# Optimization experiments

Hardware: AMD Instinct MI355X
Metric: run time of the kernel (lower is better)

The kernel has to match this reference:

```python
import jax, jax.numpy as jnp
import numpy as np

CELU_ALPHA = 3.0  # hardcoded in the torch module (nn.CELU(alpha=3.0), F.celu(alpha=3.0))

def celu(x):
    # celu(x, a) = max(0, x) + min(0, a*(exp(x/a)-1)); overflow-safe form
    return jnp.maximum(x, 0.0) + CELU_ALPHA * jnp.expm1(jnp.minimum(x, 0.0) / CELU_ALPHA)

def setup_inputs() -> dict:
    key = jax.random.key(0)
    k1, k2, k3, k4, k5 = jax.random.split(key, 5)
    N, E, H, D = 16384, 262144, 4, 64
    return {
        "features": jax.random.normal(k1, (N, D), dtype=jnp.float32),
        "metapath_embedding": jax.random.normal(k2, (E, D), dtype=jnp.float32),
        "attn1_w": jax.random.normal(k3, (H, D), dtype=jnp.float32) * 0.15,  # xavier-ish scale
        "attn2": jax.random.normal(k4, (H, D), dtype=jnp.float32) * 0.15,
        "segment_ids": jax.random.randint(k5, (E,), 0, N, dtype=jnp.int32),
    }

def reference(features, metapath_embedding, attn1_w, attn2, segment_ids):
    N, D = features.shape
    H = attn1_w.shape[0]
    # eft: same embedding broadcast over heads (torch.cat([emb]*H).view(-1,H,D))
    eft = celu(metapath_embedding)                    # [E, D]
    a1 = celu(features @ attn1_w.T)                   # [N, H] (per-node, shared across its instances)
    a2 = eft @ attn2.T                                # [E, H]
    a = celu(a1[segment_ids] + a2)                    # [E, H]
    # segment softmax over instances of each node
    m = jax.lax.stop_gradient(jax.ops.segment_max(a, segment_ids, num_segments=N))  # [N, H]
    ex = jnp.exp(a - m[segment_ids])                  # [E, H]
    denom = jax.ops.segment_sum(ex, segment_ids, num_segments=N)                    # [N, H]
    att = ex / denom[segment_ids]                     # [E, H]
    # weighted sum of eft over each node's instances -> [N, H, D]
    msg = jax.ops.segment_sum(att[:, :, None] * eft[:, None, :], segment_ids, num_segments=N)
    # empty segments yield 0 and celu(0)=0, matching the torch zero-fill branch
    return celu(msg).reshape(N, H * D)
```

## Files before the change

kernel.cpp:

```cpp
#include <hip/hip_runtime.h>
#include <math.h>

#define CAP 64
#define CSTRIDE 16

#define LOG2E    1.44269504088896341f
#define LOG2E_3  0.48089834696298780f

__device__ __forceinline__ float celu3(float x) {
    return fmaxf(x, 0.0f) + 3.0f * (exp2f(fminf(x, 0.0f) * LOG2E_3) - 1.0f);
}

template <int CTRL>
__device__ __forceinline__ float dpp_add(float v) {
    int o = __builtin_amdgcn_update_dpp(0, __float_as_int(v), CTRL, 0xf, 0xf, true);
    return v + __int_as_float(o);
}
template <int CTRL>
__device__ __forceinline__ float dpp_mov(float v) {
    int o = __builtin_amdgcn_update_dpp(0, __float_as_int(v), CTRL, 0xf, 0xf, true);
    return __int_as_float(o);
}
__device__ __forceinline__ float red16(float v) {
    v = dpp_add<0xB1>(v);
    v = dpp_add<0x4E>(v);
    v = dpp_add<0x124>(v);
    v = dpp_add<0x128>(v);
    return v;
}
__device__ __forceinline__ float wave_sum64(float v) {
    v = red16(v);
    v += __shfl_xor(v, 16, 64);
    v += __shfl_xor(v, 32, 64);
    return v;
}


__global__ __launch_bounds__(256) void init_kernel(
    int* __restrict__ counts, int N,
    const float* __restrict__ feat, const float* __restrict__ w1,
    float* __restrict__ a1)
{
    int nz = N * CSTRIDE;
    int nblk_zero = (nz + 255) / 256;
    if ((int)blockIdx.x < nblk_zero) {
        int i = blockIdx.x * 256 + threadIdx.x;
        if (i < nz) counts[i] = 0;
        return;
    }
    int n = (blockIdx.x - nblk_zero) * 4 + (threadIdx.x >> 6);
    int lane = threadIdx.x & 63;
    if (n >= N) return;
    float f = feat[(long)n * 64 + lane];
    float s[4];
#pragma unroll
    for (int h = 0; h < 4; ++h) s[h] = wave_sum64(f * w1[h * 64 + lane]);
    if (lane < 4) a1[n * 4 + lane] = celu3(s[lane]);
}


__global__ __launch_bounds__(256) void hist_kernel(
    const int* __restrict__ seg, int* __restrict__ counts,
    int* __restrict__ elist, int E)
{
    int i = blockIdx.x * 256 + threadIdx.x;
    int stride = gridDim.x * 256;
    for (; i < E; i += stride) {
        int s = seg[i];
        int r = atomicAdd(&counts[s * CSTRIDE], 1);
        if (r < CAP) elist[s * CAP + r] = i;
    }
}


__global__ __launch_bounds__(64) void fused_kernel(
    const float* __restrict__ meta, const float* __restrict__ w2,
    const float* __restrict__ a1, const int* __restrict__ counts,
    const int* __restrict__ elist, const int* __restrict__ seg,
    float* __restrict__ out, int N, int E)
{
    int lane = threadIdx.x;
    int n = blockIdx.x;
    if (n >= N) return;

    int cnt = counts[n * CSTRIDE];
    int g = lane >> 4;
    int q = lane & 15;
    int t = lane & 3;
    long ob = (long)n * 256 + g * 64 + q * 4;

    if (cnt == 0) {
        float4 z = {0.f, 0.f, 0.f, 0.f};
        *(float4*)(out + ob) = z;
        return;
    }

    float4 a1v = *(const float4*)(a1 + (long)n * 4);

    if (cnt <= CAP) {
        float4 w2q0 = *(const float4*)(w2 + 0 * 64 + q * 4);
        float4 w2q1 = *(const float4*)(w2 + 1 * 64 + q * 4);
        float4 w2q2 = *(const float4*)(w2 + 2 * 64 + q * 4);
        float4 w2q3 = *(const float4*)(w2 + 3 * 64 + q * 4);

        float a1sel = (t == 0) ? a1v.x : (t == 1) ? a1v.y : (t == 2) ? a1v.z : a1v.w;

        int eid_l = (lane < cnt) ? elist[n * CAP + lane] : 0;
        const float* meta_q = meta + q * 4;

        float sp = 0.f;
        float4 acc0 = {0,0,0,0}, acc1 = {0,0,0,0}, acc2 = {0,0,0,0}, acc3 = {0,0,0,0};

        int nch = (cnt + 3) >> 2;
#pragma unroll 8
        for (int c = 0; c < nch; ++c) {
            int j = c * 4 + g;
            bool vr = j < cnt;
            int eid = __shfl(eid_l, j);
            float4 v = *(const float4*)(meta_q + (long)eid * 64);
            float4 ef;
            ef.x = celu3(v.x); ef.y = celu3(v.y); ef.z = celu3(v.z); ef.w = celu3(v.w);

            float d0 = ef.x * w2q0.x + ef.y * w2q0.y + ef.z * w2q0.z + ef.w * w2q0.w;
            float d1 = ef.x * w2q1.x + ef.y * w2q1.y + ef.z * w2q1.z + ef.w * w2q1.w;
            float d2 = ef.x * w2q2.x + ef.y * w2q2.y + ef.z * w2q2.z + ef.w * w2q2.w;
            float d3 = ef.x * w2q3.x + ef.y * w2q3.y + ef.z * w2q3.z + ef.w * w2q3.w;

            d0 = dpp_add<0xB1>(d0); d1 = dpp_add<0xB1>(d1);
            d2 = dpp_add<0xB1>(d2); d3 = dpp_add<0xB1>(d3);
            d0 = dpp_add<0x4E>(d0); d1 = dpp_add<0x4E>(d1);
            d2 = dpp_add<0x4E>(d2); d3 = dpp_add<0x4E>(d3);
            float dsel = (t == 0) ? d0 : (t == 1) ? d1 : (t == 2) ? d2 : d3;
            dsel = dpp_add<0x124>(dsel);
            dsel = dpp_add<0x128>(dsel);

            float A = vr ? celu3(a1sel + dsel) : -INFINITY;
            float p = exp2f(fminf(A, 80.f) * LOG2E);
            sp += p;

            float b0 = dpp_mov<0x00>(p);
            float b1 = dpp_mov<0x55>(p);
            float b2 = dpp_mov<0xAA>(p);
            float b3 = dpp_mov<0xFF>(p);

            acc0.x = fmaf(b0, ef.x, acc0.x); acc0.y = fmaf(b0, ef.y, acc0.y);
            acc0.z = fmaf(b0, ef.z, acc0.z); acc0.w = fmaf(b0, ef.w, acc0.w);
            acc1.x = fmaf(b1, ef.x, acc1.x); acc1.y = fmaf(b1, ef.y, acc1.y);
            acc1.z = fmaf(b1, ef.z, acc1.z); acc1.w = fmaf(b1, ef.w, acc1.w);
            acc2.x = fmaf(b2, ef.x, acc2.x); acc2.y = fmaf(b2, ef.y, acc2.y);
            acc2.z = fmaf(b2, ef.z, acc2.z); acc2.w = fmaf(b2, ef.w, acc2.w);
            acc3.x = fmaf(b3, ef.x, acc3.x); acc3.y = fmaf(b3, ef.y, acc3.y);
            acc3.z = fmaf(b3, ef.z, acc3.z); acc3.w = fmaf(b3, ef.w, acc3.w);
        }

        sp += __shfl_xor(sp, 16); sp += __shfl_xor(sp, 32);

        acc0.x += __shfl_xor(acc0.x, 16); acc0.x += __shfl_xor(acc0.x, 32);
        acc0.y += __shfl_xor(acc0.y, 16); acc0.y += __shfl_xor(acc0.y, 32);
        acc0.z += __shfl_xor(acc0.z, 16); acc0.z += __shfl_xor(acc0.z, 32);
        acc0.w += __shfl_xor(acc0.w, 16); acc0.w += __shfl_xor(acc0.w, 32);
        acc1.x += __shfl_xor(acc1.x, 16); acc1.x += __shfl_xor(acc1.x, 32);
        acc1.y += __shfl_xor(acc1.y, 16); acc1.y += __shfl_xor(acc1.y, 32);
        acc1.z += __shfl_xor(acc1.z, 16); acc1.z += __shfl_xor(acc1.z, 32);
        acc1.w += __shfl_xor(acc1.w, 16); acc1.w += __shfl_xor(acc1.w, 32);
        acc2.x += __shfl_xor(acc2.x, 16); acc2.x += __shfl_xor(acc2.x, 32);
        acc2.y += __shfl_xor(acc2.y, 16); acc2.y += __shfl_xor(acc2.y, 32);
        acc2.z += __shfl_xor(acc2.z, 16); acc2.z += __shfl_xor(acc2.z, 32);
        acc2.w += __shfl_xor(acc2.w, 16); acc2.w += __shfl_xor(acc2.w, 32);
        acc3.x += __shfl_xor(acc3.x, 16); acc3.x += __shfl_xor(acc3.x, 32);
        acc3.y += __shfl_xor(acc3.y, 16); acc3.y += __shfl_xor(acc3.y, 32);
        acc3.z += __shfl_xor(acc3.z, 16); acc3.z += __shfl_xor(acc3.z, 32);
        acc3.w += __shfl_xor(acc3.w, 16); acc3.w += __shfl_xor(acc3.w, 32);

        float rg = 1.f / __int_as_float(__builtin_amdgcn_ds_bpermute(g << 2, __float_as_int(sp)));

        float4 av = (g == 0) ? acc0 : (g == 1) ? acc1 : (g == 2) ? acc2 : acc3;
        float4 o;
        o.x = celu3(av.x * rg); o.y = celu3(av.y * rg);
        o.z = celu3(av.z * rg); o.w = celu3(av.w * rg);
        *(float4*)(out + ob) = o;
        return;
    }

    {
        float a10 = a1v.x, a11 = a1v.y, a12 = a1v.z, a13 = a1v.w;
        float w2v0 = w2[0 * 64 + lane], w2v1 = w2[1 * 64 + lane];
        float w2v2 = w2[2 * 64 + lane], w2v3 = w2[3 * 64 + lane];
        float m0 = -INFINITY, m1 = -INFINITY, m2 = -INFINITY, m3 = -INFINITY;
        float s0 = 0.f, s1 = 0.f, s2 = 0.f, s3 = 0.f;
        float ac0 = 0.f, ac1 = 0.f, ac2 = 0.f, ac3 = 0.f;
        for (int base = 0; base < E; base += 64) {
            int e = base + lane;
            bool hit = (e < E) && (seg[e] == n);
            unsigned long long ball = __ballot(hit);
            while (ball) {
                int b = __ffsll((long long)ball) - 1;
                ball &= ball - 1;
                int eid = base + b;
                float eft = celu3(meta[(long)eid * 64 + lane]);
                float d0 = wave_sum64(eft * w2v0);
                float d1 = wave_sum64(eft * w2v1);
                float d2 = wave_sum64(eft * w2v2);
                float d3 = wave_sum64(eft * w2v3);
                float A0 = celu3(a10 + d0), A1 = celu3(a11 + d1);
                float A2 = celu3(a12 + d2), A3 = celu3(a13 + d3);
                float nm0 = fmaxf(m0, A0), nm1 = fmaxf(m1, A1);
                float nm2 = fmaxf(m2, A2), nm3 = fmaxf(m3, A3);
                float al0 = __expf(m0 - nm0), al1 = __expf(m1 - nm1);
                float al2 = __expf(m2 - nm2), al3 = __expf(m3 - nm3);
                float p0 = __expf(A0 - nm0), p1 = __expf(A1 - nm1);
                float p2 = __expf(A2 - nm2), p3 = __expf(A3 - nm3);
                s0 = fmaf(al0, s0, p0); s1 = fmaf(al1, s1, p1);
                s2 = fmaf(al2, s2, p2); s3 = fmaf(al3, s3, p3);
                ac0 = fmaf(p0, eft, al0 * ac0); ac1 = fmaf(p1, eft, al1 * ac1);
                ac2 = fmaf(p2, eft, al2 * ac2); ac3 = fmaf(p3, eft, al3 * ac3);
                m0 = nm0; m1 = nm1; m2 = nm2; m3 = nm3;
            }
        }
        long ob2 = (long)n * 256 + lane;
        out[ob2]       = celu3(ac0 / s0);
        out[ob2 + 64]  = celu3(ac1 / s1);
        out[ob2 + 128] = celu3(ac2 / s2);
        out[ob2 + 192] = celu3(ac3 / s3);
    }
}


extern "C" void kernel_launch(void* const* d_in, const int* in_sizes, int n_in,
                              void* d_out, int out_size, void* d_ws, size_t ws_size,
                              hipStream_t stream)
{
    const float* feat = (const float*)d_in[0];
    const float* meta = (const float*)d_in[1];
    const float* w1   = (const float*)d_in[2];
    const float* w2   = (const float*)d_in[3];
    const int*   seg  = (const int*)d_in[4];
    float* out = (float*)d_out;

    int N = in_sizes[0] / 64;
    int E = in_sizes[4];

    float* a1   = (float*)d_ws;
    int* counts = (int*)(a1 + (size_t)N * 4);
    int* elist  = counts + (size_t)N * CSTRIDE;

    int nblk_zero = (N * CSTRIDE + 255) / 256;
    int nblk_a1   = (N + 3) / 4;

    init_kernel<<<nblk_zero + nblk_a1, 256, 0, stream>>>(counts, N, feat, w1, a1);
    hist_kernel<<<512, 256, 0, stream>>>(seg, counts, elist, E);
    fused_kernel<<<N, 64, 0, stream>>>(meta, w2, a1, counts, elist, seg, out, N, E);
}
```

Measured before the change: 45.13 us.

## Fuse per-node attention projection into main kernel and pack counters densely

Moves the features·attn1 projection out of the init kernel and computes it inside the fused kernel, using a partial DPP reduction that leaves each lane holding its own head's sum. Counters are no longer padded to a 64-byte stride, which shrinks the zeroing pass and the histogram footprint but puts several counters in each cache line, so atomics on neighbouring nodes can contend. The fused kernel now runs four nodes per 256-thread block instead of one per 64-thread block, and the a1 workspace buffer is removed.

```diff
diff --git a/kernel.cpp b/kernel.cpp
--- a/kernel.cpp
+++ b/kernel.cpp
@@ -2,7 +2,6 @@
 #include <math.h>
 
 #define CAP 64
-#define CSTRIDE 16
 
 #define LOG2E    1.44269504088896341f
 #define LOG2E_3  0.48089834696298780f
@@ -36,26 +35,9 @@
 }
 
 
-__global__ __launch_bounds__(256) void init_kernel(
-    int* __restrict__ counts, int N,
-    const float* __restrict__ feat, const float* __restrict__ w1,
-    float* __restrict__ a1)
-{
-    int nz = N * CSTRIDE;
-    int nblk_zero = (nz + 255) / 256;
-    if ((int)blockIdx.x < nblk_zero) {
-        int i = blockIdx.x * 256 + threadIdx.x;
-        if (i < nz) counts[i] = 0;
-        return;
-    }
-    int n = (blockIdx.x - nblk_zero) * 4 + (threadIdx.x >> 6);
-    int lane = threadIdx.x & 63;
-    if (n >= N) return;
-    float f = feat[(long)n * 64 + lane];
-    float s[4];
-#pragma unroll
-    for (int h = 0; h < 4; ++h) s[h] = wave_sum64(f * w1[h * 64 + lane]);
-    if (lane < 4) a1[n * 4 + lane] = celu3(s[lane]);
+__global__ __launch_bounds__(256) void zero_kernel(int* __restrict__ p, int n) {
+    int i = blockIdx.x * 256 + threadIdx.x;
+    if (i < n) p[i] = 0;
 }
 
 
@@ -67,23 +49,24 @@
     int stride = gridDim.x * 256;
     for (; i < E; i += stride) {
         int s = seg[i];
-        int r = atomicAdd(&counts[s * CSTRIDE], 1);
+        int r = atomicAdd(&counts[s], 1);
         if (r < CAP) elist[s * CAP + r] = i;
     }
 }
 
 
-__global__ __launch_bounds__(64) void fused_kernel(
-    const float* __restrict__ meta, const float* __restrict__ w2,
-    const float* __restrict__ a1, const int* __restrict__ counts,
-    const int* __restrict__ elist, const int* __restrict__ seg,
-    float* __restrict__ out, int N, int E)
+__global__ __launch_bounds__(256) void fused_kernel(
+    const float* __restrict__ meta, const float* __restrict__ feat,
+    const float* __restrict__ w1, const float* __restrict__ w2,
+    const int* __restrict__ counts, const int* __restrict__ elist,
+    const int* __restrict__ seg, float* __restrict__ out, int N, int E)
 {
-    int lane = threadIdx.x;
-    int n = blockIdx.x;
+    int lane = threadIdx.x & 63;
+    int wv = threadIdx.x >> 6;
+    int n = blockIdx.x * 4 + wv;
     if (n >= N) return;
 
-    int cnt = counts[n * CSTRIDE];
+    int cnt = counts[n];
     int g = lane >> 4;
     int q = lane & 15;
     int t = lane & 3;
@@ -95,7 +78,22 @@
         return;
     }
 
-    float4 a1v = *(const float4*)(a1 + (long)n * 4);
+    int eid_l = (lane < cnt) ? elist[n * CAP + lane] : 0;
+
+    float f = feat[(long)n * 64 + lane];
+    float s0 = f * w1[0 * 64 + lane];
+    float s1 = f * w1[1 * 64 + lane];
+    float s2 = f * w1[2 * 64 + lane];
+    float s3 = f * w1[3 * 64 + lane];
+    s0 = dpp_add<0xB1>(s0); s1 = dpp_add<0xB1>(s1);
+    s2 = dpp_add<0xB1>(s2); s3 = dpp_add<0xB1>(s3);
+    s0 = dpp_add<0x4E>(s0); s1 = dpp_add<0x4E>(s1);
+    s2 = dpp_add<0x4E>(s2); s3 = dpp_add<0x4E>(s3);
+    float ssel = (t == 0) ? s0 : (t == 1) ? s1 : (t == 2) ? s2 : s3;
+    ssel = dpp_add<0x124>(ssel);
+    ssel = dpp_add<0x128>(ssel);
+    ssel += __shfl_xor(ssel, 16); ssel += __shfl_xor(ssel, 32);
+    float a1sel = celu3(ssel);
 
     if (cnt <= CAP) {
         float4 w2q0 = *(const float4*)(w2 + 0 * 64 + q * 4);
@@ -103,9 +101,6 @@
         float4 w2q2 = *(const float4*)(w2 + 2 * 64 + q * 4);
         float4 w2q3 = *(const float4*)(w2 + 3 * 64 + q * 4);
 
-        float a1sel = (t == 0) ? a1v.x : (t == 1) ? a1v.y : (t == 2) ? a1v.z : a1v.w;
-
-        int eid_l = (lane < cnt) ? elist[n * CAP + lane] : 0;
         const float* meta_q = meta + q * 4;
 
         float sp = 0.f;
@@ -183,7 +178,10 @@
     }
 
     {
-        float a10 = a1v.x, a11 = a1v.y, a12 = a1v.z, a13 = a1v.w;
+        float a10 = celu3(wave_sum64(f * w1[0 * 64 + lane]));
+        float a11 = celu3(wave_sum64(f * w1[1 * 64 + lane]));
+        float a12 = celu3(wave_sum64(f * w1[2 * 64 + lane]));
+        float a13 = celu3(wave_sum64(f * w1[3 * 64 + lane]));
         float w2v0 = w2[0 * 64 + lane], w2v1 = w2[1 * 64 + lane];
         float w2v2 = w2[2 * 64 + lane], w2v3 = w2[3 * 64 + lane];
         float m0 = -INFINITY, m1 = -INFINITY, m2 = -INFINITY, m3 = -INFINITY;
@@ -240,14 +238,10 @@
     int N = in_sizes[0] / 64;
     int E = in_sizes[4];
 
-    float* a1   = (float*)d_ws;
-    int* counts = (int*)(a1 + (size_t)N * 4);
-    int* elist  = counts + (size_t)N * CSTRIDE;
-
-    int nblk_zero = (N * CSTRIDE + 255) / 256;
-    int nblk_a1   = (N + 3) / 4;
-
-    init_kernel<<<nblk_zero + nblk_a1, 256, 0, stream>>>(counts, N, feat, w1, a1);
+    int* counts = (int*)d_ws;
+    int* elist  = counts + N;
+
+    zero_kernel<<<(N + 255) / 256, 256, 0, stream>>>(counts, N);
     hist_kernel<<<512, 256, 0, stream>>>(seg, counts, elist, E);
-    fused_kernel<<<N, 64, 0, stream>>>(meta, w2, a1, counts, elist, seg, out, N, E);
-}
+    fused_kernel<<<(N + 3) / 4, 256, 0, stream>>>(meta, feat, w1, w2, counts, elist, seg, out, N, E);
+}
```

Measured after the change: 47.43 us. +5.1%, slower.
